# Optimization experiments

Hardware: AMD Instinct MI355X
Metric: run time of the kernel (lower is better)

## Reference

```python
import jax, jax.numpy as jnp
import numpy as np
from jax import lax

# ---- static config (from init_kwargs / input_specs) ----
B, NB, C, F = 16, 8192, 3, 64   # batches, points-per-batch, coord dim, feat dim
RATIO, K = 0.125, 16
M = int(RATIO * NB)


def setup_inputs() -> dict:
    key = jax.random.key(0)
    kx, kp = jax.random.split(key)
    x = jax.random.normal(kx, (B * NB, F), dtype=jnp.float32)
    pos = jax.random.normal(kp, (B * NB, C), dtype=jnp.float32)
    batch = (jnp.arange(B * NB, dtype=jnp.int32) // NB).astype(jnp.int32)
    return {"x": x, "pos": pos, "batch": batch}


def _fps_single(pos_b):
    """Sequential farthest point sampling on (NB, C), deterministic start at 0.
    Returns (M,) int32 indices into pos_b."""
    n = pos_b.shape[0]

    def step(carry, _):
        min_d2, last = carry
        d2 = jnp.sum((pos_b - pos_b[last]) ** 2, axis=-1)   # (NB,)
        min_d2 = jnp.minimum(min_d2, d2)
        nxt = jnp.argmax(min_d2).astype(jnp.int32)
        return (min_d2, nxt), last

    init = (jnp.full((n,), jnp.finfo(pos_b.dtype).max, dtype=pos_b.dtype),
            jnp.int32(0))
    _, idx = lax.scan(step, init, None, length=M)
    return idx  # (M,)


def reference(x, pos, batch):
    # batch ids are block-constant (batch[i] = i // NB), so per-batch views are
    # simple reshapes -- same semantics as torch_cluster's batched fps/knn.
    pos_b = pos.reshape(B, NB, C)

    # --- farthest point sampling per batch ---
    fps_idx = jax.vmap(_fps_single)(pos_b)                            # (B, M)
    centroids = jnp.take_along_axis(pos_b, fps_idx[..., None], axis=1)  # (B, M, C)

    # --- k-NN: squared distances centroids -> all points of same batch ---
    d2 = (jnp.sum(centroids ** 2, axis=-1)[..., None]
          - 2.0 * jnp.einsum('bmc,bnc->bmn', centroids, pos_b)
          + jnp.sum(pos_b ** 2, axis=-1)[:, None, :])                 # (B, M, NB)
    _, nn_idx = lax.top_k(-d2, K)                                     # (B, M, K)

    # gather neighbor coordinates (== pos[groups_idx[1]])
    groups = jax.vmap(lambda p, i: p[i])(pos_b, nn_idx.reshape(B, M * K))  # (B, M*K, C)

    return centroids.reshape(B * M, C), groups.reshape(B * M * K, C)
```

## Files before the change

### kernel.cpp

```cpp
#include <hip/hip_runtime.h>
#include <float.h>
#include <math.h>

#define B_   16
#define NB_  8192
#define M_   1024
#define K_   16


typedef float v2f __attribute__((ext_vector_type(2)));

#define FPS_T 256
#define PPT   32
#define NPAIR (PPT/2)
#define NWAVE (FPS_T/64)

#define KNN_T   256
#define CHUNK   1024
#define GRP     8
#define BCAP    16
#define BSTRIDE 17

#define FPS_BLOCKS B_
#define WGS_PER_B  15
#define KNN_BLOCKS (B_ * WGS_PER_B)
#define MAXSP      8

__device__ __forceinline__ void topk_insert(float d2, int pi, float val[16], int idx[16])
{
    int r = 0;
    #pragma unroll
    for (int j = 0; j < 16; ++j) r += (val[j] <= d2) ? 1 : 0;
    #pragma unroll
    for (int j = 15; j >= 1; --j) {
        bool sh = (j > r);
        val[j] = sh ? val[j-1] : val[j];
        idx[j] = sh ? idx[j-1] : idx[j];
    }
    #pragma unroll
    for (int j = 0; j < 16; ++j) {
        bool pl = (j == r);
        val[j] = pl ? d2 : val[j];
        idx[j] = pl ? pi : idx[j];
    }
}

__global__ __launch_bounds__(256, 1) void fused_kernel(
    const float* __restrict__ pos, float* __restrict__ cent,
    float* __restrict__ groups, unsigned long long* __restrict__ partials,
    unsigned int* __restrict__ progress)
{
    #pragma clang fp contract(off)
    __shared__ float4 spts[NB_];
    __shared__ unsigned long long wkey[2][NWAVE];

    const int blk = blockIdx.x;
    const int t   = threadIdx.x;

    if (blk < FPS_BLOCKS) {
        const int b = blk;
        const float* pb = pos + (size_t)b * NB_ * 3;
        float* cb = cent + (size_t)b * M_ * 3;

        for (int p = t; p < NB_; p += FPS_T) {
            const float* s = pb + (size_t)p * 3;
            spts[p] = make_float4(s[0], s[1], s[2], 0.0f);
        }

        v2f px2[NPAIR], py2[NPAIR], pz2[NPAIR], md2[NPAIR];
        #pragma unroll
        for (int jj = 0; jj < NPAIR; ++jj) {
            const float* s0 = pb + (size_t)(t*PPT + 2*jj) * 3;
            px2[jj] = (v2f){s0[0], s0[3]};
            py2[jj] = (v2f){s0[1], s0[4]};
            pz2[jj] = (v2f){s0[2], s0[5]};
            md2[jj] = (v2f){FLT_MAX, FLT_MAX};
        }
        __syncthreads();

        float lx = pb[0], ly = pb[1], lz = pb[2];
        float c0x=0,c0y=0,c0z=0,c1x=0,c1y=0,c1z=0,c2x=0,c2y=0,c2z=0,c3x=0,c3y=0,c3z=0;

        for (int m = 0; m < M_; ++m) {
            if (t == (m >> 2)) {
                const int sl = m & 3;
                if      (sl == 0) { c0x=lx; c0y=ly; c0z=lz; }
                else if (sl == 1) { c1x=lx; c1y=ly; c1z=lz; }
                else if (sl == 2) { c2x=lx; c2y=ly; c2z=lz; }
                else              { c3x=lx; c3y=ly; c3z=lz; }
            }

            if ((m & 255) == 255) {
                const int cg = m >> 8;
                if ((t >> 6) == cg) {
                    float4* o = (float4*)(cb + (size_t)t * 12);
                    o[0] = make_float4(c0x, c0y, c0z, c1x);
                    o[1] = make_float4(c1y, c1z, c2x, c2y);
                    o[2] = make_float4(c2z, c3x, c3y, c3z);
                    if ((t & 63) == 0)
                        __hip_atomic_store(&progress[b], (unsigned)(cg + 1),
                                           __ATOMIC_RELEASE, __HIP_MEMORY_SCOPE_AGENT);
                }
            }
            if (m == M_ - 1) break;

            const v2f lxv = {lx,lx}, lyv = {ly,ly}, lzv = {lz,lz};
            v2f bmax2 = {-1.0f, -1.0f};
            #pragma unroll
            for (int jj = 0; jj < NPAIR; ++jj) {
                v2f dx = px2[jj] - lxv;
                v2f dy = py2[jj] - lyv;
                v2f dz = pz2[jj] - lzv;
                v2f d2 = (dx*dx + dy*dy) + dz*dz;
                v2f mj = __builtin_elementwise_min(md2[jj], d2);
                md2[jj] = mj;
                bmax2 = __builtin_elementwise_max(bmax2, mj);
            }
            float bm = fmaxf(bmax2.x, bmax2.y);

            float v = bm;
            {
                int vi;
                vi = __builtin_amdgcn_update_dpp(__float_as_int(v), __float_as_int(v), 0xB1,  0xF, 0xF, false);
                v = fmaxf(v, __int_as_float(vi));
                vi = __builtin_amdgcn_update_dpp(__float_as_int(v), __float_as_int(v), 0x4E,  0xF, 0xF, false);
                v = fmaxf(v, __int_as_float(vi));
                vi = __builtin_amdgcn_update_dpp(__float_as_int(v), __float_as_int(v), 0x141, 0xF, 0xF, false);
                v = fmaxf(v, __int_as_float(vi));
                vi = __builtin_amdgcn_update_dpp(__float_as_int(v), __float_as_int(v), 0x140, 0xF, 0xF, false);
                v = fmaxf(v, __int_as_float(vi));
                vi = __builtin_amdgcn_update_dpp(__float_as_int(v), __float_as_int(v), 0x142, 0xF, 0xF, false);
                v = fmaxf(v, __int_as_float(vi));
                vi = __builtin_amdgcn_update_dpp(__float_as_int(v), __float_as_int(v), 0x143, 0xF, 0xF, false);
                v = fmaxf(v, __int_as_float(vi));
            }
            const float wv = __int_as_float(__builtin_amdgcn_readlane(__float_as_int(v), 63));

            int jp = -1;
            #pragma unroll
            for (int jj = NPAIR - 1; jj >= 0; --jj) {
                if (md2[jj].y == wv) jp = 2*jj + 1;
                if (md2[jj].x == wv) jp = 2*jj;
            }
            const unsigned long long mk = __ballot(jp >= 0);
            const int wl = (int)__ffsll(mk) - 1;
            const int gi = __builtin_amdgcn_readlane(t*PPT + jp, wl);

            const int par = m & 1;
            if ((t & 63) == 0)
                wkey[par][t >> 6] = ((unsigned long long)__float_as_uint(wv) << 32) |
                                    (unsigned int)(~gi);
            __syncthreads();

            unsigned long long kk = wkey[par][0];
            #pragma unroll
            for (int w = 1; w < NWAVE; ++w) {
                const unsigned long long e = wkey[par][w];
                kk = (e > kk) ? e : kk;
            }
            const int best = (int)(~(unsigned int)kk);

            const float4 c = spts[best];
            lx = c.x; ly = c.y; lz = c.z;
        }
        return;
    }

    const int r = blk - FPS_BLOCKS;
    const int b = r / WGS_PER_B;
    const int w = r % WGS_PER_B;
    int cg, sp;
    if      (w == 0) { cg = 0; sp = 0; }
    else if (w < 3)  { cg = 1; sp = w - 1; }
    else if (w < 7)  { cg = 2; sp = w - 3; }
    else             { cg = 3; sp = w - 7; }
    const int span   = NB_ >> cg;
    const int pbase  = sp * span;
    const int direct = (cg == 0);
    const int nchunks = span / CHUNK;

    float4* kpts = spts;
    unsigned long long* sbuf = (unsigned long long*)(spts + CHUNK);

    const float* pb = pos + (size_t)b * NB_ * 3;

    for (int p = t; p < CHUNK; p += KNN_T) {
        const float* s = pb + (size_t)(pbase + p) * 3;
        float x = s[0], y = s[1], z = s[2];
        float pn2 = (x*x + y*y) + z*z;
        kpts[p] = make_float4(x, y, z, pn2);
    }

    if (t == 0) {
        while (__hip_atomic_load(&progress[b], __ATOMIC_ACQUIRE,
                                 __HIP_MEMORY_SCOPE_AGENT) < (unsigned)(cg + 1))
            __builtin_amdgcn_s_sleep(64);
    }
    __syncthreads();

    const int mg = b * M_ + cg * KNN_T + t;
    const float cx = cent[(size_t)mg*3+0];
    const float cy = cent[(size_t)mg*3+1];
    const float cz = cent[(size_t)mg*3+2];
    const float cn2 = (cx*cx + cy*cy) + cz*cz;

    float val[16]; int idx[16];
    #pragma unroll
    for (int j = 0; j < 16; ++j) { val[j] = FLT_MAX; idx[j] = 0; }
    float tau = FLT_MAX;
    int cnt = 0;
    unsigned long long* mybuf = sbuf + t * BSTRIDE;

    for (int c = 0; c < nchunks; ++c) {
        const int ps = pbase + c * CHUNK;

        for (int p0 = 0; p0 < CHUNK; p0 += GRP) {
            if (__any(cnt > BCAP - GRP)) {
                int n = cnt; cnt = 0;
                for (int i = 0; i < n; ++i) {
                    unsigned long long e = mybuf[i];
                    float d = __uint_as_float((unsigned int)(e >> 32));
                    int pi  = (int)(e & 0xFFFFFFFFu);
                    if (d < val[15]) topk_insert(d, pi, val, idx);
                }
                tau = val[15];
            }
            float4 q[GRP];
            #pragma unroll
            for (int i = 0; i < GRP; ++i) q[i] = kpts[p0 + i];
            float d2v[GRP];
            #pragma unroll
            for (int i = 0; i < GRP; ++i) {
                float dot = __builtin_fmaf(cz, q[i].z,
                            __builtin_fmaf(cy, q[i].y, cx * q[i].x));
                d2v[i] = (cn2 - 2.0f*dot) + q[i].w;
            }
            #pragma unroll
            for (int i = 0; i < GRP; ++i) {
                if (d2v[i] < tau) {
                    mybuf[cnt] = ((unsigned long long)__float_as_uint(d2v[i]) << 32) |
                                 (unsigned int)(ps + p0 + i);
                    ++cnt;
                }
            }
        }

        if (c + 1 < nchunks) {
            __syncthreads();
            const int ns = pbase + (c + 1) * CHUNK;
            for (int p = t; p < CHUNK; p += KNN_T) {
                const float* s = pb + (size_t)(ns + p) * 3;
                float x = s[0], y = s[1], z = s[2];
                float pn2 = (x*x + y*y) + z*z;
                kpts[p] = make_float4(x, y, z, pn2);
            }
            __syncthreads();
        }
    }
    {
        int n = cnt;
        for (int i = 0; i < n; ++i) {
            unsigned long long e = mybuf[i];
            float d = __uint_as_float((unsigned int)(e >> 32));
            int pi  = (int)(e & 0xFFFFFFFFu);
            if (d < val[15]) topk_insert(d, pi, val, idx);
        }
    }

    if (!direct) {
        unsigned long long* o = partials +
            ((((size_t)(b * 3 + (cg - 1)) * 256 + t) * MAXSP) + sp) * 16;
        #pragma unroll
        for (int kq = 0; kq < 16; ++kq)
            o[kq] = ((unsigned long long)__float_as_uint(val[kq]) << 32) | (unsigned int)idx[kq];
    } else {
        float* g = groups + (size_t)mg * K_ * 3;
        #pragma unroll
        for (int kq = 0; kq < 16; ++kq) {
            const float* s = pb + (size_t)idx[kq] * 3;
            g[kq*3+0] = s[0]; g[kq*3+1] = s[1]; g[kq*3+2] = s[2];
        }
    }
}

__global__ __launch_bounds__(256, 2) void knn_merge_c(const float* __restrict__ pos,
    const unsigned long long* __restrict__ partials, float* __restrict__ groups)
{
    const int g  = blockIdx.x * 256 + threadIdx.x;
    const int b  = g / 768;
    const int u  = g % 768;
    const int cg = 1 + u / 256;
    const int tt = u % 256;
    const int nsp = 1 << cg;
    const float* pb = pos + (size_t)b * NB_ * 3;

    const unsigned long long* base = partials +
        (((size_t)(b * 3 + (cg - 1)) * 256 + tt) * MAXSP) * 16;

    float val[16]; int idx[16];
    #pragma unroll
    for (int j = 0; j < 16; ++j) { val[j] = FLT_MAX; idx[j] = 0; }
    for (int sp = 0; sp < nsp; ++sp) {
        const unsigned long long* l = base + sp * 16;
        #pragma unroll
        for (int kq = 0; kq < 16; ++kq) {
            unsigned long long e = l[kq];
            float d = __uint_as_float((unsigned int)(e >> 32));
            int pi  = (int)(e & 0xFFFFFFFFu);
            if (d < val[15]) topk_insert(d, pi, val, idx);
        }
    }
    const int mg = b * M_ + cg * 256 + tt;
    float* o = groups + (size_t)mg * K_ * 3;
    #pragma unroll
    for (int kq = 0; kq < 16; ++kq) {
        const float* s = pb + (size_t)idx[kq] * 3;
        o[kq*3+0] = s[0]; o[kq*3+1] = s[1]; o[kq*3+2] = s[2];
    }
}

__global__ __launch_bounds__(FPS_T, 1) void fps_kernel(const float* __restrict__ pos,
                                                       float* __restrict__ cent)
{
    #pragma clang fp contract(off)
    const int b = blockIdx.x;
    const int t = threadIdx.x;
    const float* pb = pos + (size_t)b * NB_ * 3;
    float* cb = cent + (size_t)b * M_ * 3;

    __shared__ float4 spts[NB_];
    __shared__ unsigned long long wkey[2][NWAVE];

    for (int p = t; p < NB_; p += FPS_T) {
        const float* s = pb + (size_t)p * 3;
        spts[p] = make_float4(s[0], s[1], s[2], 0.0f);
    }

    v2f px2[NPAIR], py2[NPAIR], pz2[NPAIR], md2[NPAIR];
    #pragma unroll
    for (int jj = 0; jj < NPAIR; ++jj) {
        const float* s0 = pb + (size_t)(t*PPT + 2*jj) * 3;
        px2[jj] = (v2f){s0[0], s0[3]};
        py2[jj] = (v2f){s0[1], s0[4]};
        pz2[jj] = (v2f){s0[2], s0[5]};
        md2[jj] = (v2f){FLT_MAX, FLT_MAX};
    }
    __syncthreads();

    float lx = pb[0], ly = pb[1], lz = pb[2];
    float c0x=0,c0y=0,c0z=0,c1x=0,c1y=0,c1z=0,c2x=0,c2y=0,c2z=0,c3x=0,c3y=0,c3z=0;

    for (int m = 0; m < M_; ++m) {
        if (t == (m >> 2)) {
            const int sl = m & 3;
            if      (sl == 0) { c0x=lx; c0y=ly; c0z=lz; }
            else if (sl == 1) { c1x=lx; c1y=ly; c1z=lz; }
            else if (sl == 2) { c2x=lx; c2y=ly; c2z=lz; }
            else              { c3x=lx; c3y=ly; c3z=lz; }
        }
        if (m == M_ - 1) break;

        const v2f lxv = {lx,lx}, lyv = {ly,ly}, lzv = {lz,lz};
        v2f bmax2 = {-1.0f, -1.0f};
        #pragma unroll
        for (int jj = 0; jj < NPAIR; ++jj) {
            v2f dx = px2[jj] - lxv;
            v2f dy = py2[jj] - lyv;
            v2f dz = pz2[jj] - lzv;
            v2f d2 = (dx*dx + dy*dy) + dz*dz;
            v2f mj = __builtin_elementwise_min(md2[jj], d2);
            md2[jj] = mj;
            bmax2 = __builtin_elementwise_max(bmax2, mj);
        }
        float bm = fmaxf(bmax2.x, bmax2.y);

        float v = bm;
        {
            int vi;
            vi = __builtin_amdgcn_update_dpp(__float_as_int(v), __float_as_int(v), 0xB1,  0xF, 0xF, false);
            v = fmaxf(v, __int_as_float(vi));
            vi = __builtin_amdgcn_update_dpp(__float_as_int(v), __float_as_int(v), 0x4E,  0xF, 0xF, false);
            v = fmaxf(v, __int_as_float(vi));
            vi = __builtin_amdgcn_update_dpp(__float_as_int(v), __float_as_int(v), 0x141, 0xF, 0xF, false);
            v = fmaxf(v, __int_as_float(vi));
            vi = __builtin_amdgcn_update_dpp(__float_as_int(v), __float_as_int(v), 0x140, 0xF, 0xF, false);
            v = fmaxf(v, __int_as_float(vi));
            vi = __builtin_amdgcn_update_dpp(__float_as_int(v), __float_as_int(v), 0x142, 0xF, 0xF, false);
            v = fmaxf(v, __int_as_float(vi));
            vi = __builtin_amdgcn_update_dpp(__float_as_int(v), __float_as_int(v), 0x143, 0xF, 0xF, false);
            v = fmaxf(v, __int_as_float(vi));
        }
        const float wv = __int_as_float(__builtin_amdgcn_readlane(__float_as_int(v), 63));

        int jp = -1;
        #pragma unroll
        for (int jj = NPAIR - 1; jj >= 0; --jj) {
            if (md2[jj].y == wv) jp = 2*jj + 1;
            if (md2[jj].x == wv) jp = 2*jj;
        }
        const unsigned long long mk = __ballot(jp >= 0);
        const int wl = (int)__ffsll(mk) - 1;
        const int gi = __builtin_amdgcn_readlane(t*PPT + jp, wl);

        const int par = m & 1;
        if ((t & 63) == 0)
            wkey[par][t >> 6] = ((unsigned long long)__float_as_uint(wv) << 32) |
                                (unsigned int)(~gi);
        __syncthreads();

        unsigned long long kk = wkey[par][0];
        #pragma unroll
        for (int w = 1; w < NWAVE; ++w) {
            const unsigned long long e = wkey[par][w];
            kk = (e > kk) ? e : kk;
        }
        const int best = (int)(~(unsigned int)kk);

        const float4 c = spts[best];
        lx = c.x; ly = c.y; lz = c.z;
    }

    {
        float4* o = (float4*)(cb + (size_t)t * 12);
        o[0] = make_float4(c0x, c0y, c0z, c1x);
        o[1] = make_float4(c1y, c1z, c2x, c2y);
        o[2] = make_float4(c2z, c3x, c3y, c3z);
    }
}

__global__ __launch_bounds__(KNN_T, 2) void knn_kernel(const float* __restrict__ pos,
    const float* __restrict__ cent, float* __restrict__ groups,
    unsigned long long* __restrict__ partials, int nsplit)
{
    #pragma clang fp contract(off)
    __shared__ float4 kpts[CHUNK];
    __shared__ unsigned long long sbuf[KNN_T * BSTRIDE];

    const int wg = blockIdx.x;
    const int t  = threadIdx.x;
    const int per_b = 4 * nsplit;
    const int b  = wg / per_b;
    const int r  = wg % per_b;
    const int cg = r / nsplit;
    const int sp = r % nsplit;
    const int span  = NB_ / nsplit;
    const int pbase = sp * span;
    const int nchunks = span / CHUNK;

    const float* pb = pos + (size_t)b * NB_ * 3;
    const int mg = b * M_ + cg * KNN_T + t;
    const float cx = cent[(size_t)mg*3+0];
    const float cy = cent[(size_t)mg*3+1];
    const float cz = cent[(size_t)mg*3+2];
    const float cn2 = (cx*cx + cy*cy) + cz*cz;

    float val[16]; int idx[16];
    #pragma unroll
    for (int j = 0; j < 16; ++j) { val[j] = FLT_MAX; idx[j] = 0; }
    float tau = FLT_MAX;
    int cnt = 0;
    unsigned long long* mybuf = sbuf + t * BSTRIDE;

    for (int c = 0; c < nchunks; ++c) {
        const int ps = pbase + c * CHUNK;
        __syncthreads();
        for (int p = t; p < CHUNK; p += KNN_T) {
            const float* s = pb + (size_t)(ps + p) * 3;
            float x = s[0], y = s[1], z = s[2];
            float pn2 = (x*x + y*y) + z*z;
            kpts[p] = make_float4(x, y, z, pn2);
        }
        __syncthreads();

        for (int p0 = 0; p0 < CHUNK; p0 += GRP) {
            if (__any(cnt > BCAP - GRP)) {
                int n = cnt; cnt = 0;
                for (int i = 0; i < n; ++i) {
                    unsigned long long e = mybuf[i];
                    float d = __uint_as_float((unsigned int)(e >> 32));
                    int pi  = (int)(e & 0xFFFFFFFFu);
                    if (d < val[15]) topk_insert(d, pi, val, idx);
                }
                tau = val[15];
            }
            float4 q[GRP];
            #pragma unroll
            for (int i = 0; i < GRP; ++i) q[i] = kpts[p0 + i];
            float d2v[GRP];
            #pragma unroll
            for (int i = 0; i < GRP; ++i) {
                float dot = __builtin_fmaf(cz, q[i].z,
                            __builtin_fmaf(cy, q[i].y, cx * q[i].x));
                d2v[i] = (cn2 - 2.0f*dot) + q[i].w;
            }
            #pragma unroll
            for (int i = 0; i < GRP; ++i) {
                if (d2v[i] < tau) {
                    mybuf[cnt] = ((unsigned long long)__float_as_uint(d2v[i]) << 32) |
                                 (unsigned int)(ps + p0 + i);
                    ++cnt;
                }
            }
        }
    }
    {
        int n = cnt;
        for (int i = 0; i < n; ++i) {
            unsigned long long e = mybuf[i];
            float d = __uint_as_float((unsigned int)(e >> 32));
            int pi  = (int)(e & 0xFFFFFFFFu);
            if (d < val[15]) topk_insert(d, pi, val, idx);
        }
    }

    if (nsplit > 1) {
        unsigned long long* o = partials + ((size_t)mg * nsplit + sp) * 16;
        #pragma unroll
        for (int kq = 0; kq < 16; ++kq)
            o[kq] = ((unsigned long long)__float_as_uint(val[kq]) << 32) | (unsigned int)idx[kq];
    } else {
        float* g = groups + (size_t)mg * K_ * 3;
        #pragma unroll
        for (int kq = 0; kq < 16; ++kq) {
            const float* s = pb + (size_t)idx[kq] * 3;
            g[kq*3+0] = s[0]; g[kq*3+1] = s[1]; g[kq*3+2] = s[2];
        }
    }
}

__global__ __launch_bounds__(256, 2) void knn_merge(const float* __restrict__ pos,
    const unsigned long long* __restrict__ partials, float* __restrict__ groups,
    int nsplit)
{
    const int mg = blockIdx.x * 256 + threadIdx.x;
    const int b  = mg >> 10;
    const float* pb = pos + (size_t)b * NB_ * 3;

    float val[16]; int idx[16];
    #pragma unroll
    for (int j = 0; j < 16; ++j) { val[j] = FLT_MAX; idx[j] = 0; }
    for (int sp = 0; sp < nsplit; ++sp) {
        const unsigned long long* l = partials + ((size_t)mg * nsplit + sp) * 16;
        #pragma unroll
        for (int kq = 0; kq < 16; ++kq) {
            unsigned long long e = l[kq];
            float d = __uint_as_float((unsigned int)(e >> 32));
            int pi  = (int)(e & 0xFFFFFFFFu);
            if (d < val[15]) topk_insert(d, pi, val, idx);
        }
    }
    float* g = groups + (size_t)mg * K_ * 3;
    #pragma unroll
    for (int kq = 0; kq < 16; ++kq) {
        const float* s = pb + (size_t)idx[kq] * 3;
        g[kq*3+0] = s[0]; g[kq*3+1] = s[1]; g[kq*3+2] = s[2];
    }
}

extern "C" void kernel_launch(void* const* d_in, const int* in_sizes, int n_in,
                              void* d_out, int out_size, void* d_ws, size_t ws_size,
                              hipStream_t stream)
{
    (void)in_sizes; (void)n_in; (void)out_size;
    const float* pos = (const float*)d_in[1];
    float* out    = (float*)d_out;
    float* cent   = out;
    float* groups = out + (size_t)B_ * M_ * 3;

    const size_t FLAGS = 256;
    const size_t PART  = (size_t)B_ * 768 * MAXSP * 16 * sizeof(unsigned long long);

    if (ws_size >= FLAGS + PART) {
        unsigned int* progress = (unsigned int*)d_ws;
        unsigned long long* partials = (unsigned long long*)((char*)d_ws + FLAGS);

        hipMemsetAsync(d_ws, 0, FLAGS, stream);

        fused_kernel<<<FPS_BLOCKS + KNN_BLOCKS, 256, 0, stream>>>(pos, cent, groups,
                                                                  partials, progress);
        knn_merge_c<<<(B_ * 768) / 256, 256, 0, stream>>>(pos, partials, groups);
    } else {
        fps_kernel<<<B_, FPS_T, 0, stream>>>(pos, cent);
        const size_t lst = (size_t)B_ * M_ * 16 * sizeof(unsigned long long);
        int nsplit = (ws_size >= 8*lst) ? 8 : (ws_size >= 4*lst) ? 4 :
                     (ws_size >= 2*lst) ? 2 : 1;
        knn_kernel<<<B_ * 4 * nsplit, KNN_T, 0, stream>>>(pos, cent, groups,
                                                          (unsigned long long*)d_ws, nsplit);
        if (nsplit > 1)
            knn_merge<<<(B_ * M_) / 256, 256, 0, stream>>>(pos,
                (const unsigned long long*)d_ws, groups, nsplit);
    }
}
```

Baseline: 1.267 ms.

## Fold kNN partial merge into fused kernel via last-block counter, vectorize loads

Removes the separate knn_merge_c launch. Each split block now writes its partial top-k, increments an atomic counter, and the last block to finish for a chunk group does the merge and gathers the coordinates. The point loads in both the FPS and kNN paths are vectorized to float4 triples. A 64-point warm-up seeds the kNN threshold before filtering begins, and the candidate-buffer append is made branchless. The cost is extra fences and atomics, plus a merge tail that runs inside the persistent kernel. The float4 loads assume the input is 16-byte aligned.

New measurement: 1.270 ms. Within noise of the previous version (+0.2%).

```diff
diff --git a/kernel.cpp b/kernel.cpp
--- a/kernel.cpp
+++ b/kernel.cpp
@@ -20,6 +20,7 @@
 #define GRP     8
 #define BCAP    16
 #define BSTRIDE 17
+#define WARM    64
 
 #define FPS_BLOCKS B_
 #define WGS_PER_B  15
@@ -62,19 +63,30 @@
         const float* pb = pos + (size_t)b * NB_ * 3;
         float* cb = cent + (size_t)b * M_ * 3;
 
-        for (int p = t; p < NB_; p += FPS_T) {
-            const float* s = pb + (size_t)p * 3;
-            spts[p] = make_float4(s[0], s[1], s[2], 0.0f);
+        {
+            const float4* src = (const float4*)pb;
+            for (int g = t; g < NB_/4; g += FPS_T) {
+                float4 f0 = src[3*g+0], f1 = src[3*g+1], f2 = src[3*g+2];
+                spts[4*g+0] = make_float4(f0.x, f0.y, f0.z, 0.0f);
+                spts[4*g+1] = make_float4(f0.w, f1.x, f1.y, 0.0f);
+                spts[4*g+2] = make_float4(f1.z, f1.w, f2.x, 0.0f);
+                spts[4*g+3] = make_float4(f2.y, f2.z, f2.w, 0.0f);
+            }
         }
 
         v2f px2[NPAIR], py2[NPAIR], pz2[NPAIR], md2[NPAIR];
         #pragma unroll
-        for (int jj = 0; jj < NPAIR; ++jj) {
-            const float* s0 = pb + (size_t)(t*PPT + 2*jj) * 3;
-            px2[jj] = (v2f){s0[0], s0[3]};
-            py2[jj] = (v2f){s0[1], s0[4]};
-            pz2[jj] = (v2f){s0[2], s0[5]};
-            md2[jj] = (v2f){FLT_MAX, FLT_MAX};
+        for (int ga = 0; ga < NPAIR/2; ++ga) {
+            const float4* s4 = (const float4*)(pb + (size_t)(t*PPT + 4*ga) * 3);
+            float4 f0 = s4[0], f1 = s4[1], f2 = s4[2];
+            px2[2*ga]   = (v2f){f0.x, f0.w};
+            py2[2*ga]   = (v2f){f0.y, f1.x};
+            pz2[2*ga]   = (v2f){f0.z, f1.y};
+            px2[2*ga+1] = (v2f){f1.z, f2.y};
+            py2[2*ga+1] = (v2f){f1.w, f2.z};
+            pz2[2*ga+1] = (v2f){f2.x, f2.w};
+            md2[2*ga]   = (v2f){FLT_MAX, FLT_MAX};
+            md2[2*ga+1] = (v2f){FLT_MAX, FLT_MAX};
         }
         __syncthreads();
 
@@ -184,11 +196,17 @@
 
     const float* pb = pos + (size_t)b * NB_ * 3;
 
-    for (int p = t; p < CHUNK; p += KNN_T) {
-        const float* s = pb + (size_t)(pbase + p) * 3;
-        float x = s[0], y = s[1], z = s[2];
-        float pn2 = (x*x + y*y) + z*z;
-        kpts[p] = make_float4(x, y, z, pn2);
+    {
+        const float4* src = (const float4*)(pb + (size_t)pbase * 3);
+        float4 f0 = src[3*t+0], f1 = src[3*t+1], f2 = src[3*t+2];
+        float x0=f0.x, y0=f0.y, z0=f0.z;
+        float x1=f0.w, y1=f1.x, z1=f1.y;
+        float x2=f1.z, y2=f1.w, z2=f2.x;
+        float x3=f2.y, y3=f2.z, z3=f2.w;
+        kpts[4*t+0] = make_float4(x0, y0, z0, (x0*x0 + y0*y0) + z0*z0);
+        kpts[4*t+1] = make_float4(x1, y1, z1, (x1*x1 + y1*y1) + z1*z1);
+        kpts[4*t+2] = make_float4(x2, y2, z2, (x2*x2 + y2*y2) + z2*z2);
+        kpts[4*t+3] = make_float4(x3, y3, z3, (x3*x3 + y3*y3) + z3*z3);
     }
 
     if (t == 0) {
@@ -207,14 +225,22 @@
     float val[16]; int idx[16];
     #pragma unroll
     for (int j = 0; j < 16; ++j) { val[j] = FLT_MAX; idx[j] = 0; }
-    float tau = FLT_MAX;
     int cnt = 0;
     unsigned long long* mybuf = sbuf + t * BSTRIDE;
 
+    for (int p = 0; p < WARM; ++p) {
+        float4 q = kpts[p];
+        float dot = __builtin_fmaf(cz, q.z, __builtin_fmaf(cy, q.y, cx * q.x));
+        float d2 = (cn2 - 2.0f*dot) + q.w;
+        if (d2 < val[15]) topk_insert(d2, pbase + p, val, idx);
+    }
+    float tau = val[15];
+
+    int pstart = WARM;
     for (int c = 0; c < nchunks; ++c) {
         const int ps = pbase + c * CHUNK;
 
-        for (int p0 = 0; p0 < CHUNK; p0 += GRP) {
+        for (int p0 = pstart; p0 < CHUNK; p0 += GRP) {
             if (__any(cnt > BCAP - GRP)) {
                 int n = cnt; cnt = 0;
                 for (int i = 0; i < n; ++i) {
@@ -237,23 +263,26 @@
             }
             #pragma unroll
             for (int i = 0; i < GRP; ++i) {
-                if (d2v[i] < tau) {
-                    mybuf[cnt] = ((unsigned long long)__float_as_uint(d2v[i]) << 32) |
-                                 (unsigned int)(ps + p0 + i);
-                    ++cnt;
-                }
-            }
-        }
+                mybuf[cnt] = ((unsigned long long)__float_as_uint(d2v[i]) << 32) |
+                             (unsigned int)(ps + p0 + i);
+                cnt += (d2v[i] < tau) ? 1 : 0;
+            }
+        }
+        pstart = 0;
 
         if (c + 1 < nchunks) {
             __syncthreads();
             const int ns = pbase + (c + 1) * CHUNK;
-            for (int p = t; p < CHUNK; p += KNN_T) {
-                const float* s = pb + (size_t)(ns + p) * 3;
-                float x = s[0], y = s[1], z = s[2];
-                float pn2 = (x*x + y*y) + z*z;
-                kpts[p] = make_float4(x, y, z, pn2);
-            }
+            const float4* src = (const float4*)(pb + (size_t)ns * 3);
+            float4 f0 = src[3*t+0], f1 = src[3*t+1], f2 = src[3*t+2];
+            float x0=f0.x, y0=f0.y, z0=f0.z;
+            float x1=f0.w, y1=f1.x, z1=f1.y;
+            float x2=f1.z, y2=f1.w, z2=f2.x;
+            float x3=f2.y, y3=f2.z, z3=f2.w;
+            kpts[4*t+0] = make_float4(x0, y0, z0, (x0*x0 + y0*y0) + z0*z0);
+            kpts[4*t+1] = make_float4(x1, y1, z1, (x1*x1 + y1*y1) + z1*z1);
+            kpts[4*t+2] = make_float4(x2, y2, z2, (x2*x2 + y2*y2) + z2*z2);
+            kpts[4*t+3] = make_float4(x3, y3, z3, (x3*x3 + y3*y3) + z3*z3);
             __syncthreads();
         }
     }
@@ -267,55 +296,55 @@
         }
     }
 
-    if (!direct) {
-        unsigned long long* o = partials +
-            ((((size_t)(b * 3 + (cg - 1)) * 256 + t) * MAXSP) + sp) * 16;
-        #pragma unroll
-        for (int kq = 0; kq < 16; ++kq)
-            o[kq] = ((unsigned long long)__float_as_uint(val[kq]) << 32) | (unsigned int)idx[kq];
-    } else {
+    if (direct) {
         float* g = groups + (size_t)mg * K_ * 3;
         #pragma unroll
         for (int kq = 0; kq < 16; ++kq) {
             const float* s = pb + (size_t)idx[kq] * 3;
             g[kq*3+0] = s[0]; g[kq*3+1] = s[1]; g[kq*3+2] = s[2];
         }
-    }
-}
-
-__global__ __launch_bounds__(256, 2) void knn_merge_c(const float* __restrict__ pos,
-    const unsigned long long* __restrict__ partials, float* __restrict__ groups)
-{
-    const int g  = blockIdx.x * 256 + threadIdx.x;
-    const int b  = g / 768;
-    const int u  = g % 768;
-    const int cg = 1 + u / 256;
-    const int tt = u % 256;
-    const int nsp = 1 << cg;
-    const float* pb = pos + (size_t)b * NB_ * 3;
-
-    const unsigned long long* base = partials +
-        (((size_t)(b * 3 + (cg - 1)) * 256 + tt) * MAXSP) * 16;
-
-    float val[16]; int idx[16];
-    #pragma unroll
-    for (int j = 0; j < 16; ++j) { val[j] = FLT_MAX; idx[j] = 0; }
-    for (int sp = 0; sp < nsp; ++sp) {
-        const unsigned long long* l = base + sp * 16;
+        return;
+    }
+
+    const int cidx = b * 3 + (cg - 1);
+    const int nsp  = 1 << cg;
+    {
+        unsigned long long* o = partials + (((size_t)cidx * 256 + t) * MAXSP + sp) * 16;
+        #pragma unroll
+        for (int kq = 0; kq < 16; ++kq)
+            o[kq] = ((unsigned long long)__float_as_uint(val[kq]) << 32) | (unsigned int)idx[kq];
+    }
+    __threadfence();
+    __syncthreads();
+    unsigned int* counters = progress + 16;
+    if (t == 0)
+        wkey[0][0] = (unsigned long long)atomicAdd(&counters[cidx], 1u);
+    __syncthreads();
+    if ((unsigned)wkey[0][0] != (unsigned)(nsp - 1))
+        return;
+
+    __threadfence();
+    {
+        float mval[16]; int midx[16];
+        #pragma unroll
+        for (int j = 0; j < 16; ++j) { mval[j] = FLT_MAX; midx[j] = 0; }
+        const unsigned long long* base2 = partials + (((size_t)cidx * 256 + t) * MAXSP) * 16;
+        for (int s2 = 0; s2 < nsp; ++s2) {
+            const unsigned long long* l = base2 + s2 * 16;
+            #pragma unroll
+            for (int kq = 0; kq < 16; ++kq) {
+                unsigned long long e = l[kq];
+                float d = __uint_as_float((unsigned int)(e >> 32));
+                int pi  = (int)(e & 0xFFFFFFFFu);
+                if (d < mval[15]) topk_insert(d, pi, mval, midx);
+            }
+        }
+        float* g = groups + (size_t)mg * K_ * 3;
         #pragma unroll
         for (int kq = 0; kq < 16; ++kq) {
-            unsigned long long e = l[kq];
-            float d = __uint_as_float((unsigned int)(e >> 32));
-            int pi  = (int)(e & 0xFFFFFFFFu);
-            if (d < val[15]) topk_insert(d, pi, val, idx);
-        }
-    }
-    const int mg = b * M_ + cg * 256 + tt;
-    float* o = groups + (size_t)mg * K_ * 3;
-    #pragma unroll
-    for (int kq = 0; kq < 16; ++kq) {
-        const float* s = pb + (size_t)idx[kq] * 3;
-        o[kq*3+0] = s[0]; o[kq*3+1] = s[1]; o[kq*3+2] = s[2];
+            const float* s = pb + (size_t)midx[kq] * 3;
+            g[kq*3+0] = s[0]; g[kq*3+1] = s[1]; g[kq*3+2] = s[2];
+        }
     }
 }
 
@@ -578,7 +607,6 @@
 
         fused_kernel<<<FPS_BLOCKS + KNN_BLOCKS, 256, 0, stream>>>(pos, cent, groups,
                                                                   partials, progress);
-        knn_merge_c<<<(B_ * 768) / 256, 256, 0, stream>>>(pos, partials, groups);
     } else {
         fps_kernel<<<B_, FPS_T, 0, stream>>>(pos, cent);
         const size_t lst = (size_t)B_ * M_ * 16 * sizeof(unsigned long long);
```

## Fold kNN partial merge into fused kernel via last-arriver counter; use packed FP32 asm

Applied to the files above, without the earlier changes.

Removes the separate knn_merge_c launch. Each split workgroup writes its partial top-k lists, bumps an atomic counter per (batch, centroid group), and the last workgroup to arrive merges all partials and gathers the neighbor coordinates. This saves one kernel launch and lets the merge overlap with the FPS tail. The FPS distance loop also uses inline v_pk_add/v_pk_mul asm so packed FP32 math is guaranteed, with the counters placed in the already-zeroed flags area.

Result: slower. 1.341 ms (+5.8%).

```diff
diff --git a/kernel.cpp b/kernel.cpp
--- a/kernel.cpp
+++ b/kernel.cpp
@@ -9,6 +9,22 @@
 
 
 typedef float v2f __attribute__((ext_vector_type(2)));
+
+__device__ __forceinline__ v2f pk_sub(v2f a, v2f b) {
+    v2f r;
+    asm("v_pk_add_f32 %0, %1, %2 neg_lo:[0,1] neg_hi:[0,1]" : "=v"(r) : "v"(a), "v"(b));
+    return r;
+}
+__device__ __forceinline__ v2f pk_mul(v2f a, v2f b) {
+    v2f r;
+    asm("v_pk_mul_f32 %0, %1, %2" : "=v"(r) : "v"(a), "v"(b));
+    return r;
+}
+__device__ __forceinline__ v2f pk_add(v2f a, v2f b) {
+    v2f r;
+    asm("v_pk_add_f32 %0, %1, %2" : "=v"(r) : "v"(a), "v"(b));
+    return r;
+}
 
 #define FPS_T 256
 #define PPT   32
@@ -45,7 +61,7 @@
     }
 }
 
-__global__ __launch_bounds__(256, 1) void fused_kernel(
+__global__ __launch_bounds__(FPS_T, 1) void fused_kernel(
     const float* __restrict__ pos, float* __restrict__ cent,
     float* __restrict__ groups, unsigned long long* __restrict__ partials,
     unsigned int* __restrict__ progress)
@@ -108,10 +124,10 @@
             v2f bmax2 = {-1.0f, -1.0f};
             #pragma unroll
             for (int jj = 0; jj < NPAIR; ++jj) {
-                v2f dx = px2[jj] - lxv;
-                v2f dy = py2[jj] - lyv;
-                v2f dz = pz2[jj] - lzv;
-                v2f d2 = (dx*dx + dy*dy) + dz*dz;
+                v2f dx = pk_sub(px2[jj], lxv);
+                v2f dy = pk_sub(py2[jj], lyv);
+                v2f dz = pk_sub(pz2[jj], lzv);
+                v2f d2 = pk_add(pk_add(pk_mul(dx,dx), pk_mul(dy,dy)), pk_mul(dz,dz));
                 v2f mj = __builtin_elementwise_min(md2[jj], d2);
                 md2[jj] = mj;
                 bmax2 = __builtin_elementwise_max(bmax2, mj);
@@ -267,55 +283,56 @@
         }
     }
 
-    if (!direct) {
-        unsigned long long* o = partials +
-            ((((size_t)(b * 3 + (cg - 1)) * 256 + t) * MAXSP) + sp) * 16;
-        #pragma unroll
-        for (int kq = 0; kq < 16; ++kq)
-            o[kq] = ((unsigned long long)__float_as_uint(val[kq]) << 32) | (unsigned int)idx[kq];
-    } else {
+    if (direct) {
         float* g = groups + (size_t)mg * K_ * 3;
         #pragma unroll
         for (int kq = 0; kq < 16; ++kq) {
             const float* s = pb + (size_t)idx[kq] * 3;
             g[kq*3+0] = s[0]; g[kq*3+1] = s[1]; g[kq*3+2] = s[2];
         }
-    }
-}
-
-__global__ __launch_bounds__(256, 2) void knn_merge_c(const float* __restrict__ pos,
-    const unsigned long long* __restrict__ partials, float* __restrict__ groups)
-{
-    const int g  = blockIdx.x * 256 + threadIdx.x;
-    const int b  = g / 768;
-    const int u  = g % 768;
-    const int cg = 1 + u / 256;
-    const int tt = u % 256;
-    const int nsp = 1 << cg;
-    const float* pb = pos + (size_t)b * NB_ * 3;
-
-    const unsigned long long* base = partials +
-        (((size_t)(b * 3 + (cg - 1)) * 256 + tt) * MAXSP) * 16;
-
-    float val[16]; int idx[16];
-    #pragma unroll
-    for (int j = 0; j < 16; ++j) { val[j] = FLT_MAX; idx[j] = 0; }
-    for (int sp = 0; sp < nsp; ++sp) {
-        const unsigned long long* l = base + sp * 16;
+        return;
+    }
+
+    const int cidx = b * 3 + (cg - 1);
+    const int nsp  = 1 << cg;
+    {
+        unsigned long long* o = partials + (((size_t)cidx * 256 + t) * MAXSP + sp) * 16;
+        #pragma unroll
+        for (int kq = 0; kq < 16; ++kq)
+            o[kq] = ((unsigned long long)__float_as_uint(val[kq]) << 32) | (unsigned int)idx[kq];
+    }
+    __syncthreads();
+    unsigned int* counters = progress + 16;
+    if (t == 0) {
+        __threadfence();
+        wkey[0][0] = (unsigned long long)atomicAdd(&counters[cidx], 1u);
+    }
+    __syncthreads();
+    if ((unsigned)wkey[0][0] != (unsigned)(nsp - 1))
+        return;
+
+    __threadfence();
+    {
+        float mval[16]; int midx[16];
+        #pragma unroll
+        for (int j = 0; j < 16; ++j) { mval[j] = FLT_MAX; midx[j] = 0; }
+        const unsigned long long* base2 = partials + (((size_t)cidx * 256 + t) * MAXSP) * 16;
+        for (int s2 = 0; s2 < nsp; ++s2) {
+            const unsigned long long* l = base2 + s2 * 16;
+            #pragma unroll
+            for (int kq = 0; kq < 16; ++kq) {
+                unsigned long long e = l[kq];
+                float d = __uint_as_float((unsigned int)(e >> 32));
+                int pi  = (int)(e & 0xFFFFFFFFu);
+                if (d < mval[15]) topk_insert(d, pi, mval, midx);
+            }
+        }
+        float* g = groups + (size_t)mg * K_ * 3;
         #pragma unroll
         for (int kq = 0; kq < 16; ++kq) {
-            unsigned long long e = l[kq];
-            float d = __uint_as_float((unsigned int)(e >> 32));
-            int pi  = (int)(e & 0xFFFFFFFFu);
-            if (d < val[15]) topk_insert(d, pi, val, idx);
-        }
-    }
-    const int mg = b * M_ + cg * 256 + tt;
-    float* o = groups + (size_t)mg * K_ * 3;
-    #pragma unroll
-    for (int kq = 0; kq < 16; ++kq) {
-        const float* s = pb + (size_t)idx[kq] * 3;
-        o[kq*3+0] = s[0]; o[kq*3+1] = s[1]; o[kq*3+2] = s[2];
+            const float* s = pb + (size_t)midx[kq] * 3;
+            g[kq*3+0] = s[0]; g[kq*3+1] = s[1]; g[kq*3+2] = s[2];
+        }
     }
 }
 
@@ -576,9 +593,8 @@
 
         hipMemsetAsync(d_ws, 0, FLAGS, stream);
 
-        fused_kernel<<<FPS_BLOCKS + KNN_BLOCKS, 256, 0, stream>>>(pos, cent, groups,
-                                                                  partials, progress);
-        knn_merge_c<<<(B_ * 768) / 256, 256, 0, stream>>>(pos, partials, groups);
+        fused_kernel<<<FPS_BLOCKS + KNN_BLOCKS, FPS_T, 0, stream>>>(pos, cent, groups,
+                                                                    partials, progress);
     } else {
         fps_kernel<<<B_, FPS_T, 0, stream>>>(pos, cent);
         const size_t lst = (size_t)B_ * M_ * 16 * sizeof(unsigned long long);
```
